# Performance work log

Hardware: AMD Instinct MI355X
Metric: run time of the kernel (lower is better)

The kernel has to match this reference:

```python
import jax, jax.numpy as jnp
import numpy as np

N_NODES = 100000
N_EDGES = 1600000
N_GRAPHS = 64
IN_DIM, HID_DIM, OUT_DIM = 128, 256, 256


def setup_inputs() -> dict:
    key = jax.random.key(0)
    ks = jax.random.split(key, 7)
    x = jax.random.normal(ks[0], (N_NODES, IN_DIM), dtype=jnp.float32)
    edge_index = jax.random.randint(ks[1], (2, N_EDGES), 0, N_NODES, dtype=jnp.int32)
    batch = jnp.sort(jax.random.randint(ks[2], (N_NODES,), 0, N_GRAPHS, dtype=jnp.int32))
    # Glorot-style init for GCN linear weights, zero bias (as in PyG defaults)
    W1 = jax.random.normal(ks[3], (IN_DIM, HID_DIM), dtype=jnp.float32) / np.sqrt(IN_DIM)
    b1 = jnp.zeros((HID_DIM,), dtype=jnp.float32)
    W2 = jax.random.normal(ks[4], (HID_DIM, OUT_DIM), dtype=jnp.float32) / np.sqrt(HID_DIM)
    b2 = jnp.zeros((OUT_DIM,), dtype=jnp.float32)
    return {"x": x, "edge_index": edge_index, "batch": batch,
            "W1": W1, "b1": b1, "W2": W2, "b2": b2}


def reference(x, edge_index, batch, W1, b1, W2, b2):
    N = x.shape[0]
    # --- GCN normalization with self-loops (computed once, edge structure fixed) ---
    loops = jnp.arange(N, dtype=edge_index.dtype)
    row = jnp.concatenate([edge_index[0], loops])  # source nodes  [E+N]
    col = jnp.concatenate([edge_index[1], loops])  # target nodes  [E+N]
    deg = jax.ops.segment_sum(jnp.ones_like(col, dtype=x.dtype), col, num_segments=N)
    dinv = jax.lax.rsqrt(jnp.maximum(deg, 1.0))    # deg >= 1 due to self-loops
    norm = dinv[row] * dinv[col]                   # [E+N]

    def gcn_conv(h, W, b):
        h = h @ W                                  # linear transform first (PyG order)
        msg = h[row] * norm[:, None]               # gather + normalize  [E+N, D]
        agg = jax.ops.segment_sum(msg, col, num_segments=N)  # scatter-add
        return agg + b

    h = jax.nn.relu(gcn_conv(x, W1, b1))
    h = jax.nn.relu(gcn_conv(h, W2, b2))

    # --- global mean pool over graph ids ---
    s = jax.ops.segment_sum(h, batch, num_segments=N_GRAPHS)           # [G, D]
    cnt = jax.ops.segment_sum(jnp.ones((N, 1), h.dtype), batch, num_segments=N_GRAPHS)
    return s / jnp.maximum(cnt, 1.0)
```

## Files before the change

kernel.cpp:

```cpp
#include <hip/hip_runtime.h>

typedef __attribute__((ext_vector_type(8))) short short8;
typedef __attribute__((ext_vector_type(4))) float float4v;

#define CAP 64

__device__ __forceinline__ ushort f2bf(float f) {
    uint u = __float_as_uint(f);
    u += 0x7fffu + ((u >> 16) & 1u);
    return (ushort)(u >> 16);
}
__device__ __forceinline__ float bf2f(ushort h) {
    return __uint_as_float((uint)h << 16);
}
__device__ __forceinline__ void acc8(float* acc, uint4 v) {
    acc[0] += __uint_as_float(v.x << 16);
    acc[1] += __uint_as_float(v.x & 0xffff0000u);
    acc[2] += __uint_as_float(v.y << 16);
    acc[3] += __uint_as_float(v.y & 0xffff0000u);
    acc[4] += __uint_as_float(v.z << 16);
    acc[5] += __uint_as_float(v.z & 0xffff0000u);
    acc[6] += __uint_as_float(v.w << 16);
    acc[7] += __uint_as_float(v.w & 0xffff0000u);
}
__device__ __forceinline__ int clampi(int v, int n) {
    return (int)min((uint)v, (uint)(n - 1));
}

__global__ void zero_all_k(int* __restrict__ idg, float* __restrict__ out,
                           int n, int nout) {
    int i = blockIdx.x * 256 + threadIdx.x;
    if (i < n) idg[i] = 0;
    if (i < nout) out[i] = 0.f;
}

__global__ void fill_k(const int* __restrict__ row, const int* __restrict__ col,
                       int* __restrict__ idg, int* __restrict__ eidx, int E) {
    int e = blockIdx.x * 256 + threadIdx.x;
    if (e < E) {
        int c = col[e];
        int p = atomicAdd(&idg[c], 1);
        if (p < CAP) eidx[(size_t)c * CAP + p] = row[e];
    }
}

__global__ void prep_k(const float* __restrict__ W1, ushort* __restrict__ W1p,
                       const float* __restrict__ W2, ushort* __restrict__ W2p,
                       const float* __restrict__ x, const int* __restrict__ idg,
                       ushort* __restrict__ xb, int n4) {
    int idx = blockIdx.x * 256 + threadIdx.x;
    if (idx < 32768) {
        int j = idx & 7, lane = (idx >> 3) & 63;
        int s = (idx >> 9) % 4, nt = (idx >> 9) / 4;
        int k = 32 * s + (lane >> 4) * 8 + j;
        int c = nt * 16 + (lane & 15);
        W1p[idx] = f2bf(W1[k * 256 + c]);
    } else if (idx < 32768 + 65536) {
        int q = idx - 32768;
        int j = q & 7, lane = (q >> 3) & 63;
        int s = (q >> 9) % 8, nt = (q >> 9) / 8;
        int k = 32 * s + (lane >> 4) * 8 + j;
        int c = nt * 16 + (lane & 15);
        W2p[q] = f2bf(W2[k * 256 + c]);
    } else {
        int i = idx - (32768 + 65536);
        if (i < n4) {
            int node = i >> 5;
            float di = rsqrtf((float)(idg[node] + 1));
            float4 v = ((const float4*)x)[i];
            ushort4 o;
            o.x = f2bf(v.x * di); o.y = f2bf(v.y * di);
            o.z = f2bf(v.z * di); o.w = f2bf(v.w * di);
            ((ushort4*)xb)[i] = o;
        }
    }
}

__global__ __launch_bounds__(256) void agg128_k(const ushort* __restrict__ g,
                                                ushort* __restrict__ out,
                                                const int* __restrict__ idg,
                                                const int* __restrict__ eidx, int n) {
    int w = threadIdx.x >> 6, lane = threadIdx.x & 63;
    int i = blockIdx.x * 4 + w;
    if (i >= n) return;
    int q = lane >> 4, sub = lane & 15;
    float acc[8] = {};
    if (q == 0) {
        uint4 v = *(const uint4*)(g + (size_t)i * 128 + sub * 8);
        acc8(acc, v);
    }
    int deg = idg[i];
    int cnt = min(deg, CAP);
    const int* ep = eidx + (size_t)i * CAP;
    int j = q;
    for (; j + 12 < cnt; j += 16) {
        int sA = clampi(ep[j], n),     sB = clampi(ep[j + 4], n);
        int sC = clampi(ep[j + 8], n), sD = clampi(ep[j + 12], n);
        uint4 vA = *(const uint4*)(g + (size_t)sA * 128 + sub * 8);
        uint4 vB = *(const uint4*)(g + (size_t)sB * 128 + sub * 8);
        uint4 vC = *(const uint4*)(g + (size_t)sC * 128 + sub * 8);
        uint4 vD = *(const uint4*)(g + (size_t)sD * 128 + sub * 8);
        acc8(acc, vA); acc8(acc, vB); acc8(acc, vC); acc8(acc, vD);
    }
    for (; j < cnt; j += 4) {
        int sA = clampi(ep[j], n);
        uint4 vA = *(const uint4*)(g + (size_t)sA * 128 + sub * 8);
        acc8(acc, vA);
    }
#pragma unroll
    for (int d = 0; d < 8; ++d) {
        acc[d] += __shfl_xor(acc[d], 16);
        acc[d] += __shfl_xor(acc[d], 32);
    }
    if (q == 0) {
        float di = rsqrtf((float)(deg + 1));
        uint4 o;
        o.x = (uint)f2bf(acc[0] * di) | ((uint)f2bf(acc[1] * di) << 16);
        o.y = (uint)f2bf(acc[2] * di) | ((uint)f2bf(acc[3] * di) << 16);
        o.z = (uint)f2bf(acc[4] * di) | ((uint)f2bf(acc[5] * di) << 16);
        o.w = (uint)f2bf(acc[6] * di) | ((uint)f2bf(acc[7] * di) << 16);
        *(uint4*)(out + (size_t)i * 128 + sub * 8) = o;
    }
}

__global__ __launch_bounds__(256) void agg256_k(const ushort* __restrict__ g,
                                                ushort* __restrict__ out,
                                                const int* __restrict__ idg,
                                                const int* __restrict__ eidx, int n) {
    int w = threadIdx.x >> 6, lane = threadIdx.x & 63;
    int i = blockIdx.x * 4 + w;
    if (i >= n) return;
    int half = lane >> 5, sub = lane & 31;
    float acc[8] = {};
    if (half == 0) {
        uint4 v = *(const uint4*)(g + (size_t)i * 256 + sub * 8);
        acc8(acc, v);
    }
    int deg = idg[i];
    int cnt = min(deg, CAP);
    const int* ep = eidx + (size_t)i * CAP;
    int j = half;
    for (; j + 6 < cnt; j += 8) {
        int sA = clampi(ep[j], n),     sB = clampi(ep[j + 2], n);
        int sC = clampi(ep[j + 4], n), sD = clampi(ep[j + 6], n);
        uint4 vA = *(const uint4*)(g + (size_t)sA * 256 + sub * 8);
        uint4 vB = *(const uint4*)(g + (size_t)sB * 256 + sub * 8);
        uint4 vC = *(const uint4*)(g + (size_t)sC * 256 + sub * 8);
        uint4 vD = *(const uint4*)(g + (size_t)sD * 256 + sub * 8);
        acc8(acc, vA); acc8(acc, vB); acc8(acc, vC); acc8(acc, vD);
    }
    for (; j < cnt; j += 2) {
        int sA = clampi(ep[j], n);
        uint4 vA = *(const uint4*)(g + (size_t)sA * 256 + sub * 8);
        acc8(acc, vA);
    }
#pragma unroll
    for (int d = 0; d < 8; ++d) acc[d] += __shfl_xor(acc[d], 32);
    if (half == 0) {
        float di = rsqrtf((float)(deg + 1));
        uint4 o;
        o.x = (uint)f2bf(acc[0] * di) | ((uint)f2bf(acc[1] * di) << 16);
        o.y = (uint)f2bf(acc[2] * di) | ((uint)f2bf(acc[3] * di) << 16);
        o.z = (uint)f2bf(acc[4] * di) | ((uint)f2bf(acc[5] * di) << 16);
        o.w = (uint)f2bf(acc[6] * di) | ((uint)f2bf(acc[7] * di) << 16);
        *(uint4*)(out + (size_t)i * 256 + sub * 8) = o;
    }
}

template <int K, bool SCALE>
__global__ __launch_bounds__(256) void gemm_ldsw_k(const ushort* __restrict__ A,
                                                   const ushort* __restrict__ Wp,
                                                   const float* __restrict__ bias,
                                                   const int* __restrict__ idg,
                                                   ushort* __restrict__ C, int M) {
    constexpr int S = K / 32;
    constexpr int STAGE_US = 4 * S * 64 * 8;
    __shared__ ushort ldsW[STAGE_US];
    int tid = threadIdx.x, wv = tid >> 6, lane = tid & 63;
    int quad = lane >> 4, l15 = lane & 15;
    int rowBase = blockIdx.x * 64 + wv * 16;
    int arow = rowBase + l15; if (arow > M - 1) arow = M - 1;
    const ushort* abase = A + (size_t)arow * K + quad * 8;
    short8 af[S];
#pragma unroll
    for (int s = 0; s < S; ++s) af[s] = *(const short8*)(abase + 32 * s);

    float diRow[4];
    if (SCALE) {
#pragma unroll
        for (int r = 0; r < 4; ++r) {
            int rr = min(rowBase + quad * 4 + r, M - 1);
            diRow[r] = rsqrtf((float)(idg[rr] + 1));
        }
    }

#pragma unroll
    for (int st = 0; st < 4; ++st) {
        __syncthreads();
        {
            const uint4* src = (const uint4*)(Wp + (size_t)st * STAGE_US);
            uint4* dst = (uint4*)ldsW;
#pragma unroll
            for (int it = 0; it < STAGE_US / 8 / 256; ++it)
                dst[it * 256 + tid] = src[it * 256 + tid];
        }
        __syncthreads();
        float4v acc[4];
#pragma unroll
        for (int nt = 0; nt < 4; ++nt) {
            float4v a = {0.f, 0.f, 0.f, 0.f};
#pragma unroll
            for (int s = 0; s < S; ++s) {
                short8 bf = *(const short8*)&ldsW[((nt * S + s) * 64 + lane) * 8];
                a = __builtin_amdgcn_mfma_f32_16x16x32_bf16(af[s], bf, a, 0, 0, 0);
            }
            acc[nt] = a;
        }
#pragma unroll
        for (int nt = 0; nt < 4; ++nt) {
            int col = (st * 4 + nt) * 16 + l15;
            float b = bias[col];
#pragma unroll
            for (int r = 0; r < 4; ++r) {
                int row = rowBase + quad * 4 + r;
                if (row < M) {
                    float v = fmaxf(acc[nt][r] + b, 0.f);
                    if (SCALE) v *= diRow[r];
                    C[(size_t)row * 256 + col] = f2bf(v);
                }
            }
        }
    }
}

__global__ void pool_k(const ushort* __restrict__ h, const int* __restrict__ batch,
                       float* __restrict__ outsum, int n) {
    int d = threadIdx.x;
    int n0 = blockIdx.x * 128;
    int n1 = min(n0 + 128, n);
    int gcur = -1;
    float sum = 0.f;
    for (int nn = n0; nn < n1; ++nn) {
        int g = batch[nn] & 63;
        float v = bf2f(h[(size_t)nn * 256 + d]);
        if (g != gcur) {
            if (gcur >= 0) atomicAdd(&outsum[gcur * 256 + d], sum);
            gcur = g;
            sum = v;
        } else {
            sum += v;
        }
    }
    if (gcur >= 0) atomicAdd(&outsum[gcur * 256 + d], sum);
}

__global__ void final_k(float* __restrict__ out, const int* __restrict__ batch, int n) {
    __shared__ float cntS;
    int g = blockIdx.x, d = threadIdx.x;
    if (d == 0) {
        int lo = 0, hi = n;
        while (lo < hi) { int mid = (lo + hi) >> 1; if (batch[mid] < g) lo = mid + 1; else hi = mid; }
        int s = lo;
        lo = 0; hi = n;
        int g1 = g + 1;
        while (lo < hi) { int mid = (lo + hi) >> 1; if (batch[mid] < g1) lo = mid + 1; else hi = mid; }
        cntS = (float)(lo - s);
    }
    __syncthreads();
    out[g * 256 + d] /= fmaxf(cntS, 1.0f);
}

extern "C" void kernel_launch(void* const* d_in, const int* in_sizes, int n_in,
                              void* d_out, int out_size, void* d_ws, size_t ws_size,
                              hipStream_t stream) {
    const float* x  = (const float*)d_in[0];
    const int*   ei = (const int*)d_in[1];
    const int*   batch = (const int*)d_in[2];
    const float* W1 = (const float*)d_in[3];
    const float* b1 = (const float*)d_in[4];
    const float* W2 = (const float*)d_in[5];
    const float* b2 = (const float*)d_in[6];
    float* out = (float*)d_out;

    const int N  = in_sizes[2];
    const int E  = in_sizes[1] / 2;
    const int* row = ei;
    const int* col = ei + E;

    char* p = (char*)d_ws;
    auto alloc = [&](size_t bytes) {
        char* q = p;
        p += (bytes + 255) & ~(size_t)255;
        return q;
    };
    int*    idg    = (int*)alloc((size_t)N * 4);
    int*    eidx   = (int*)alloc((size_t)N * CAP * 4);
    ushort* W1p    = (ushort*)alloc(16 * 4 * 64 * 8 * 2);
    ushort* W2p    = (ushort*)alloc(16 * 8 * 64 * 8 * 2);
    ushort* xb     = (ushort*)alloc((size_t)N * 128 * 2);
    ushort* aggX   = (ushort*)alloc((size_t)N * 128 * 2);
    ushort* g1     = (ushort*)alloc((size_t)N * 256 * 2);
    ushort* aggH   = (ushort*)alloc((size_t)N * 256 * 2);
    ushort* h2     = (ushort*)alloc((size_t)N * 256 * 2);

    const int nb  = (N + 255) / 256;
    const int ebl = (E + 255) / 256;

    zero_all_k<<<nb, 256, 0, stream>>>(idg, out, N, out_size);

    fill_k<<<ebl, 256, 0, stream>>>(row, col, idg, eidx, E);

    const int n4 = N * 32;
    prep_k<<<(98304 + n4 + 255) / 256, 256, 0, stream>>>(W1, W1p, W2, W2p, x, idg, xb, n4);

    agg128_k<<<(N + 3) / 4, 256, 0, stream>>>(xb, aggX, idg, eidx, N);
    const int gb = (N + 63) / 64;
    gemm_ldsw_k<128, true><<<gb, 256, 0, stream>>>(aggX, W1p, b1, idg, g1, N);

    agg256_k<<<(N + 3) / 4, 256, 0, stream>>>(g1, aggH, idg, eidx, N);
    gemm_ldsw_k<256, false><<<gb, 256, 0, stream>>>(aggH, W2p, b2, nullptr, h2, N);

    pool_k<<<(N + 127) / 128, 256, 0, stream>>>(h2, batch, out, N);
    final_k<<<64, 256, 0, stream>>>(out, batch, N);
}
```

Baseline: 527.8 us.

## Bin edges by destination block before building per-node adjacency lists

Replaces the single scatter pass that atomically appends each edge to its target's adjacency slot with a two-pass binning scheme. The first pass groups edges into per-chunk bins of 128 destination nodes. The second pass has one block per bin insert the grouped edges, so the atomics and eidx writes stay local. This aims to cut random atomic and write traffic across the 25.6MB eidx array, at the cost of an extra kernel and extra bin-buffer traffic. The bin buffer reuses the h2 buffer, and edges that overflow a bin fall back to the direct path.

```diff
diff --git a/kernel.cpp b/kernel.cpp
--- a/kernel.cpp
+++ b/kernel.cpp
@@ -4,6 +4,9 @@
 typedef __attribute__((ext_vector_type(4))) float float4v;
 
 #define CAP 64
+#define NPB 128
+#define NCHUNK 8
+#define BINCAP 384
 
 __device__ __forceinline__ ushort f2bf(float f) {
     uint u = __float_as_uint(f);
@@ -28,19 +31,47 @@
 }
 
 __global__ void zero_all_k(int* __restrict__ idg, float* __restrict__ out,
-                           int n, int nout) {
+                           int* __restrict__ binCnt, int n, int nout, int nbc) {
     int i = blockIdx.x * 256 + threadIdx.x;
     if (i < n) idg[i] = 0;
     if (i < nout) out[i] = 0.f;
-}
-
-__global__ void fill_k(const int* __restrict__ row, const int* __restrict__ col,
-                       int* __restrict__ idg, int* __restrict__ eidx, int E) {
+    if (i < nbc) binCnt[i] = 0;
+}
+
+__global__ void fillbin1_k(const int* __restrict__ row, const int* __restrict__ col,
+                           int* __restrict__ idg, int* __restrict__ eidx,
+                           int* __restrict__ binCnt, int2* __restrict__ binBuf,
+                           int E, int nbins) {
     int e = blockIdx.x * 256 + threadIdx.x;
+    int chunk = blockIdx.x & (NCHUNK - 1);
     if (e < E) {
-        int c = col[e];
+        int c = col[e], r = row[e];
+        int b = c >> 7;
+        int cell = chunk * nbins + b;
+        int p = atomicAdd(&binCnt[cell], 1);
+        if (p < BINCAP) {
+            binBuf[(size_t)cell * BINCAP + p] = make_int2(r, c);
+        } else {
+            int q = atomicAdd(&idg[c], 1);
+            if (q < CAP) eidx[(size_t)c * CAP + q] = r;
+        }
+    }
+}
+
+__global__ __launch_bounds__(512) void fillbin2_k(const int* __restrict__ binCnt,
+                                                  const int2* __restrict__ binBuf,
+                                                  int* __restrict__ idg,
+                                                  int* __restrict__ eidx, int nbins) {
+    int bin = blockIdx.x;
+    int wv = threadIdx.x >> 6, lane = threadIdx.x & 63;
+    int cell = wv * nbins + bin;
+    int n = min(binCnt[cell], BINCAP);
+    const int2* bp = binBuf + (size_t)cell * BINCAP;
+    for (int j = lane; j < n; j += 64) {
+        int2 pr = bp[j];
+        int c = pr.y;
         int p = atomicAdd(&idg[c], 1);
-        if (p < CAP) eidx[(size_t)c * CAP + p] = row[e];
+        if (p < CAP) eidx[(size_t)c * CAP + p] = pr.x;
     }
 }
 
@@ -303,12 +334,18 @@
     ushort* aggH   = (ushort*)alloc((size_t)N * 256 * 2);
     ushort* h2     = (ushort*)alloc((size_t)N * 256 * 2);
 
+    const int nbins = (N + NPB - 1) >> 7;
+    const int nbc   = NCHUNK * nbins;
+    int*    binCnt = (int*)alloc((size_t)nbc * 4);
+    int2*   binBuf = (int2*)h2;
+
     const int nb  = (N + 255) / 256;
     const int ebl = (E + 255) / 256;
 
-    zero_all_k<<<nb, 256, 0, stream>>>(idg, out, N, out_size);
-
-    fill_k<<<ebl, 256, 0, stream>>>(row, col, idg, eidx, E);
+    zero_all_k<<<nb, 256, 0, stream>>>(idg, out, binCnt, N, out_size, nbc);
+
+    fillbin1_k<<<ebl, 256, 0, stream>>>(row, col, idg, eidx, binCnt, binBuf, E, nbins);
+    fillbin2_k<<<nbins, 512, 0, stream>>>(binCnt, binBuf, idg, eidx, nbins);
 
     const int n4 = N * 32;
     prep_k<<<(98304 + n4 + 255) / 256, 256, 0, stream>>>(W1, W1p, W2, W2p, x, idg, xb, n4);
```

Result: slower. 542.3 us (+2.8%).

## Fuse neighbor aggregation into MFMA GEMM and replicate degree counters for CSR build

Applied to the files above, without the earlier changes.

Merges each layer's gather-sum aggregation into the GEMM kernel. Each lane now accumulates the neighbor rows for its own A-fragment row directly in registers, so the aggregated intermediates are never written to or read back from global memory. The edge-bucket build is split into count, scan and place passes, with NREP replicated atomic counters to reduce atomic contention. The cost is that each lane gathers whole row fragments serially per neighbor, giving less memory-level parallelism per wave. It also adds two extra small kernels and uses per-edge rank bytes.

```diff
diff --git a/kernel.cpp b/kernel.cpp
--- a/kernel.cpp
+++ b/kernel.cpp
@@ -2,8 +2,10 @@
 
 typedef __attribute__((ext_vector_type(8))) short short8;
 typedef __attribute__((ext_vector_type(4))) float float4v;
+typedef __attribute__((ext_vector_type(4))) uint uint4v;
 
 #define CAP 64
+#define NREP 8
 
 __device__ __forceinline__ ushort f2bf(float f) {
     uint u = __float_as_uint(f);
@@ -27,20 +29,49 @@
     return (int)min((uint)v, (uint)(n - 1));
 }
 
-__global__ void zero_all_k(int* __restrict__ idg, float* __restrict__ out,
-                           int n, int nout) {
+__global__ void zero_all_k(int* __restrict__ cnt, float* __restrict__ out,
+                           int ncnt, int nout) {
     int i = blockIdx.x * 256 + threadIdx.x;
-    if (i < n) idg[i] = 0;
+    if (i < ncnt) cnt[i] = 0;
     if (i < nout) out[i] = 0.f;
 }
 
-__global__ void fill_k(const int* __restrict__ row, const int* __restrict__ col,
-                       int* __restrict__ idg, int* __restrict__ eidx, int E) {
+__global__ void count_k(const int* __restrict__ col, int* __restrict__ cnt,
+                        unsigned char* __restrict__ rank, int E, int N) {
     int e = blockIdx.x * 256 + threadIdx.x;
+    int r = blockIdx.x & (NREP - 1);
     if (e < E) {
         int c = col[e];
-        int p = atomicAdd(&idg[c], 1);
-        if (p < CAP) eidx[(size_t)c * CAP + p] = row[e];
+        int p = atomicAdd(&cnt[(size_t)r * N + c], 1);
+        rank[e] = (unsigned char)min(p, 255);
+    }
+}
+
+__global__ void scan_k(const int* __restrict__ cnt, int* __restrict__ idg,
+                       unsigned long long* __restrict__ bases, int N) {
+    int v = blockIdx.x * 256 + threadIdx.x;
+    if (v >= N) return;
+    int deg = 0;
+    unsigned long long pk = 0;
+#pragma unroll
+    for (int r = 0; r < NREP; ++r) {
+        pk |= (unsigned long long)min(deg, 255) << (8 * r);
+        deg += cnt[(size_t)r * N + v];
+    }
+    idg[v] = deg;
+    bases[v] = pk;
+}
+
+__global__ void place_k(const int* __restrict__ row, const int* __restrict__ col,
+                        const unsigned char* __restrict__ rank,
+                        const unsigned long long* __restrict__ bases,
+                        int* __restrict__ eidx, int E) {
+    int e = blockIdx.x * 256 + threadIdx.x;
+    int r = blockIdx.x & (NREP - 1);
+    if (e < E) {
+        int c = col[e];
+        int slot = (int)((bases[c] >> (8 * r)) & 255) + (int)rank[e];
+        if (slot < CAP) eidx[(size_t)c * CAP + slot] = row[e];
     }
 }
 
@@ -76,117 +107,69 @@
     }
 }
 
-__global__ __launch_bounds__(256) void agg128_k(const ushort* __restrict__ g,
-                                                ushort* __restrict__ out,
-                                                const int* __restrict__ idg,
-                                                const int* __restrict__ eidx, int n) {
-    int w = threadIdx.x >> 6, lane = threadIdx.x & 63;
-    int i = blockIdx.x * 4 + w;
-    if (i >= n) return;
-    int q = lane >> 4, sub = lane & 15;
-    float acc[8] = {};
-    if (q == 0) {
-        uint4 v = *(const uint4*)(g + (size_t)i * 128 + sub * 8);
-        acc8(acc, v);
-    }
-    int deg = idg[i];
-    int cnt = min(deg, CAP);
-    const int* ep = eidx + (size_t)i * CAP;
-    int j = q;
-    for (; j + 12 < cnt; j += 16) {
-        int sA = clampi(ep[j], n),     sB = clampi(ep[j + 4], n);
-        int sC = clampi(ep[j + 8], n), sD = clampi(ep[j + 12], n);
-        uint4 vA = *(const uint4*)(g + (size_t)sA * 128 + sub * 8);
-        uint4 vB = *(const uint4*)(g + (size_t)sB * 128 + sub * 8);
-        uint4 vC = *(const uint4*)(g + (size_t)sC * 128 + sub * 8);
-        uint4 vD = *(const uint4*)(g + (size_t)sD * 128 + sub * 8);
-        acc8(acc, vA); acc8(acc, vB); acc8(acc, vC); acc8(acc, vD);
-    }
-    for (; j < cnt; j += 4) {
-        int sA = clampi(ep[j], n);
-        uint4 vA = *(const uint4*)(g + (size_t)sA * 128 + sub * 8);
-        acc8(acc, vA);
-    }
-#pragma unroll
-    for (int d = 0; d < 8; ++d) {
-        acc[d] += __shfl_xor(acc[d], 16);
-        acc[d] += __shfl_xor(acc[d], 32);
-    }
-    if (q == 0) {
-        float di = rsqrtf((float)(deg + 1));
-        uint4 o;
-        o.x = (uint)f2bf(acc[0] * di) | ((uint)f2bf(acc[1] * di) << 16);
-        o.y = (uint)f2bf(acc[2] * di) | ((uint)f2bf(acc[3] * di) << 16);
-        o.z = (uint)f2bf(acc[4] * di) | ((uint)f2bf(acc[5] * di) << 16);
-        o.w = (uint)f2bf(acc[6] * di) | ((uint)f2bf(acc[7] * di) << 16);
-        *(uint4*)(out + (size_t)i * 128 + sub * 8) = o;
-    }
-}
-
-__global__ __launch_bounds__(256) void agg256_k(const ushort* __restrict__ g,
-                                                ushort* __restrict__ out,
-                                                const int* __restrict__ idg,
-                                                const int* __restrict__ eidx, int n) {
-    int w = threadIdx.x >> 6, lane = threadIdx.x & 63;
-    int i = blockIdx.x * 4 + w;
-    if (i >= n) return;
-    int half = lane >> 5, sub = lane & 31;
-    float acc[8] = {};
-    if (half == 0) {
-        uint4 v = *(const uint4*)(g + (size_t)i * 256 + sub * 8);
-        acc8(acc, v);
-    }
-    int deg = idg[i];
-    int cnt = min(deg, CAP);
-    const int* ep = eidx + (size_t)i * CAP;
-    int j = half;
-    for (; j + 6 < cnt; j += 8) {
-        int sA = clampi(ep[j], n),     sB = clampi(ep[j + 2], n);
-        int sC = clampi(ep[j + 4], n), sD = clampi(ep[j + 6], n);
-        uint4 vA = *(const uint4*)(g + (size_t)sA * 256 + sub * 8);
-        uint4 vB = *(const uint4*)(g + (size_t)sB * 256 + sub * 8);
-        uint4 vC = *(const uint4*)(g + (size_t)sC * 256 + sub * 8);
-        uint4 vD = *(const uint4*)(g + (size_t)sD * 256 + sub * 8);
-        acc8(acc, vA); acc8(acc, vB); acc8(acc, vC); acc8(acc, vD);
-    }
-    for (; j < cnt; j += 2) {
-        int sA = clampi(ep[j], n);
-        uint4 vA = *(const uint4*)(g + (size_t)sA * 256 + sub * 8);
-        acc8(acc, vA);
-    }
-#pragma unroll
-    for (int d = 0; d < 8; ++d) acc[d] += __shfl_xor(acc[d], 32);
-    if (half == 0) {
-        float di = rsqrtf((float)(deg + 1));
-        uint4 o;
-        o.x = (uint)f2bf(acc[0] * di) | ((uint)f2bf(acc[1] * di) << 16);
-        o.y = (uint)f2bf(acc[2] * di) | ((uint)f2bf(acc[3] * di) << 16);
-        o.z = (uint)f2bf(acc[4] * di) | ((uint)f2bf(acc[5] * di) << 16);
-        o.w = (uint)f2bf(acc[6] * di) | ((uint)f2bf(acc[7] * di) << 16);
-        *(uint4*)(out + (size_t)i * 256 + sub * 8) = o;
-    }
-}
-
-template <int K, bool SCALE>
-__global__ __launch_bounds__(256) void gemm_ldsw_k(const ushort* __restrict__ A,
-                                                   const ushort* __restrict__ Wp,
-                                                   const float* __restrict__ bias,
-                                                   const int* __restrict__ idg,
-                                                   ushort* __restrict__ C, int M) {
+template <int K, bool SCALE_C>
+__global__ __launch_bounds__(256) void fused_k(const ushort* __restrict__ g,
+                                               const ushort* __restrict__ Wp,
+                                               const float* __restrict__ bias,
+                                               const int* __restrict__ idg,
+                                               const int* __restrict__ eidx,
+                                               ushort* __restrict__ C, int M) {
     constexpr int S = K / 32;
     constexpr int STAGE_US = 4 * S * 64 * 8;
     __shared__ ushort ldsW[STAGE_US];
     int tid = threadIdx.x, wv = tid >> 6, lane = tid & 63;
     int quad = lane >> 4, l15 = lane & 15;
     int rowBase = blockIdx.x * 64 + wv * 16;
-    int arow = rowBase + l15; if (arow > M - 1) arow = M - 1;
-    const ushort* abase = A + (size_t)arow * K + quad * 8;
+    int arow = min(rowBase + l15, M - 1);
+
+    float acc[S * 8] = {};
+    {
+        const ushort* rp = g + (size_t)arow * K + quad * 8;
+#pragma unroll
+        for (int s = 0; s < S; ++s) {
+            uint4 v = *(const uint4*)(rp + 32 * s);
+            acc8(acc + 8 * s, v);
+        }
+    }
+    int deg = idg[arow];
+    int cnt = min(deg, CAP);
+    const int* ep = eidx + (size_t)arow * CAP;
+    int j = 0;
+    if (K == 128) {
+        for (; j + 2 <= cnt; j += 2) {
+            int sA = clampi(__builtin_nontemporal_load(ep + j), M);
+            int sB = clampi(__builtin_nontemporal_load(ep + j + 1), M);
+            const ushort* pA = g + (size_t)sA * K + quad * 8;
+            const ushort* pB = g + (size_t)sB * K + quad * 8;
+            uint4 vA[S], vB[S];
+#pragma unroll
+            for (int s = 0; s < S; ++s) { vA[s] = *(const uint4*)(pA + 32 * s); }
+#pragma unroll
+            for (int s = 0; s < S; ++s) { vB[s] = *(const uint4*)(pB + 32 * s); }
+#pragma unroll
+            for (int s = 0; s < S; ++s) { acc8(acc + 8 * s, vA[s]); acc8(acc + 8 * s, vB[s]); }
+        }
+    }
+    for (; j < cnt; ++j) {
+        int sA = clampi(__builtin_nontemporal_load(ep + j), M);
+        const ushort* pA = g + (size_t)sA * K + quad * 8;
+        uint4 vA[S];
+#pragma unroll
+        for (int s = 0; s < S; ++s) { vA[s] = *(const uint4*)(pA + 32 * s); }
+#pragma unroll
+        for (int s = 0; s < S; ++s) { acc8(acc + 8 * s, vA[s]); }
+    }
+
+    float dia = rsqrtf((float)(deg + 1));
     short8 af[S];
 #pragma unroll
-    for (int s = 0; s < S; ++s) af[s] = *(const short8*)(abase + 32 * s);
+    for (int s = 0; s < S; ++s) {
+#pragma unroll
+        for (int t = 0; t < 8; ++t) af[s][t] = (short)f2bf(acc[8 * s + t] * dia);
+    }
 
     float diRow[4];
-    if (SCALE) {
+    if (SCALE_C) {
 #pragma unroll
         for (int r = 0; r < 4; ++r) {
             int rr = min(rowBase + quad * 4 + r, M - 1);
@@ -205,7 +188,7 @@
                 dst[it * 256 + tid] = src[it * 256 + tid];
         }
         __syncthreads();
-        float4v acc[4];
+        float4v accd[4];
 #pragma unroll
         for (int nt = 0; nt < 4; ++nt) {
             float4v a = {0.f, 0.f, 0.f, 0.f};
@@ -214,7 +197,7 @@
                 short8 bf = *(const short8*)&ldsW[((nt * S + s) * 64 + lane) * 8];
                 a = __builtin_amdgcn_mfma_f32_16x16x32_bf16(af[s], bf, a, 0, 0, 0);
             }
-            acc[nt] = a;
+            accd[nt] = a;
         }
 #pragma unroll
         for (int nt = 0; nt < 4; ++nt) {
@@ -222,11 +205,11 @@
             float b = bias[col];
 #pragma unroll
             for (int r = 0; r < 4; ++r) {
-                int row = rowBase + quad * 4 + r;
-                if (row < M) {
-                    float v = fmaxf(acc[nt][r] + b, 0.f);
-                    if (SCALE) v *= diRow[r];
-                    C[(size_t)row * 256 + col] = f2bf(v);
+                int rw = rowBase + quad * 4 + r;
+                if (rw < M) {
+                    float v = fmaxf(accd[nt][r] + b, 0.f);
+                    if (SCALE_C) v *= diRow[r];
+                    C[(size_t)rw * 256 + col] = f2bf(v);
                 }
             }
         }
@@ -298,27 +281,29 @@
     ushort* W1p    = (ushort*)alloc(16 * 4 * 64 * 8 * 2);
     ushort* W2p    = (ushort*)alloc(16 * 8 * 64 * 8 * 2);
     ushort* xb     = (ushort*)alloc((size_t)N * 128 * 2);
-    ushort* aggX   = (ushort*)alloc((size_t)N * 128 * 2);
     ushort* g1     = (ushort*)alloc((size_t)N * 256 * 2);
-    ushort* aggH   = (ushort*)alloc((size_t)N * 256 * 2);
     ushort* h2     = (ushort*)alloc((size_t)N * 256 * 2);
-
+    int*    cnt    = (int*)alloc((size_t)NREP * N * 4);
+    unsigned char* rank = (unsigned char*)alloc((size_t)E);
+    unsigned long long* bases = (unsigned long long*)alloc((size_t)N * 8);
+
+    const int ncnt = NREP * N;
+    const int zb  = (ncnt + 255) / 256;
     const int nb  = (N + 255) / 256;
     const int ebl = (E + 255) / 256;
 
-    zero_all_k<<<nb, 256, 0, stream>>>(idg, out, N, out_size);
-
-    fill_k<<<ebl, 256, 0, stream>>>(row, col, idg, eidx, E);
+    zero_all_k<<<zb, 256, 0, stream>>>(cnt, out, ncnt, out_size);
+
+    count_k<<<ebl, 256, 0, stream>>>(col, cnt, rank, E, N);
+    scan_k<<<nb, 256, 0, stream>>>(cnt, idg, bases, N);
+    place_k<<<ebl, 256, 0, stream>>>(row, col, rank, bases, eidx, E);
 
     const int n4 = N * 32;
     prep_k<<<(98304 + n4 + 255) / 256, 256, 0, stream>>>(W1, W1p, W2, W2p, x, idg, xb, n4);
 
-    agg128_k<<<(N + 3) / 4, 256, 0, stream>>>(xb, aggX, idg, eidx, N);
     const int gb = (N + 63) / 64;
-    gemm_ldsw_k<128, true><<<gb, 256, 0, stream>>>(aggX, W1p, b1, idg, g1, N);
-
-    agg256_k<<<(N + 3) / 4, 256, 0, stream>>>(g1, aggH, idg, eidx, N);
-    gemm_ldsw_k<256, false><<<gb, 256, 0, stream>>>(aggH, W2p, b2, nullptr, h2, N);
+    fused_k<128, true><<<gb, 256, 0, stream>>>(xb, W1p, b1, idg, eidx, g1, N);
+    fused_k<256, false><<<gb, 256, 0, stream>>>(g1, W2p, b2, idg, eidx, h2, N);
 
     pool_k<<<(N + 127) / 128, 256, 0, stream>>>(h2, batch, out, N);
     final_k<<<64, 256, 0, stream>>>(out, batch, N);
```

Result: slower. 595.4 us (+12.8%).
